# Performance work log

Measured on AMD Instinct MI355X. Metric: run time of the kernel, lower is better.

The kernel has to match this reference:

```python
import jax, jax.numpy as jnp
import numpy as np
from jax import lax

F = 64          # nb_filters
K_DOWN = 4      # size_kernel_sample
K_RES = 3       # size_kernel_res
DIL = 3         # rate_dilation_res
N_DOWN = 3      # downsampling blocks (one level)
N_RES = 4       # residual sub-blocks per block
N_EMB = 512     # codebook size
BETA = 0.25


def conv1d(x, w, b, stride=1, dil=1, act=True):
    # x: (B,T,C), w: (K,Cin,Cout)
    y = lax.conv_general_dilated(x, w, (stride,), 'SAME', rhs_dilation=(dil,),
                                 dimension_numbers=('NWC', 'WIO', 'NWC')) + b
    return jax.nn.relu(y) if act else y


def conv1d_t(x, w, b, stride):
    # transposed conv, w: (K, Cin, Cout)
    y = lax.conv_transpose(x, w, (stride,), 'SAME',
                           dimension_numbers=('NWC', 'WIO', 'NWC')) + b
    return jax.nn.relu(y)


def setup_inputs() -> dict:
    key = jax.random.key(0)
    ks = jax.random.split(key, 12)
    s_in = 1.0 / np.sqrt(K_DOWN * 1)
    s_f = 1.0 / np.sqrt(K_DOWN * F)
    s_r = 1.0 / np.sqrt(K_RES * F)
    return {
        'x': jax.random.normal(ks[0], (4, 65536, 1), dtype=jnp.float32),
        'w_down0': jax.random.normal(ks[1], (K_DOWN, 1, F), dtype=jnp.float32) * s_in,
        'b_down0': jnp.zeros((F,), jnp.float32),
        'w_down': jax.random.normal(ks[2], (N_DOWN - 1, K_DOWN, F, F), dtype=jnp.float32) * s_f,
        'b_down': jnp.zeros((N_DOWN - 1, F), jnp.float32),
        'w_res_enc': jax.random.normal(ks[3], (N_DOWN, N_RES, 2, K_RES, F, F), dtype=jnp.float32) * s_r,
        'b_res_enc': jnp.zeros((N_DOWN, N_RES, 2, F), jnp.float32),
        'codebook': jax.random.normal(ks[4], (N_EMB, F), dtype=jnp.float32),
        'w_res_dec': jax.random.normal(ks[5], (N_DOWN, N_RES, 2, K_RES, F, F), dtype=jnp.float32) * s_r,
        'b_res_dec': jnp.zeros((N_DOWN, N_RES, 2, F), jnp.float32),
        'w_up': jax.random.normal(ks[6], (N_DOWN, K_DOWN, F, F), dtype=jnp.float32) * s_f,
        'b_up': jnp.zeros((N_DOWN, F), jnp.float32),
        'w_proj': jax.random.normal(ks[7], (K_RES, F, 1), dtype=jnp.float32) * s_r,
        'b_proj': jnp.zeros((1,), jnp.float32),
    }


def reference(x, w_down0, b_down0, w_down, b_down, w_res_enc, b_res_enc,
              codebook, w_res_dec, b_res_dec, w_up, b_up, w_proj, b_proj):
    # ---- Encoder: N_DOWN stride-2 downsampling blocks, each followed by
    # N_RES ForwardResidualSubBlocks (dilated conv -> conv, residual add) ----
    h = conv1d(x, w_down0, b_down0, stride=2)
    for blk in range(N_DOWN):
        if blk > 0:
            h = conv1d(h, w_down[blk - 1], b_down[blk - 1], stride=2)
        for r in range(N_RES):
            y = conv1d(h, w_res_enc[blk, r, 0], b_res_enc[blk, r, 0], dil=DIL)
            y = conv1d(y, w_res_enc[blk, r, 1], b_res_enc[blk, r, 1], dil=1)
            h = h + y
    z_e = h  # (B, T/8, F)

    # ---- VectorQuantiser over channel axis ----
    dot = jnp.einsum('btd,kd->btk', z_e, codebook)          # tensordot
    nz = jnp.sum(jnp.square(z_e), axis=-1, keepdims=True)   # (B,T,1)
    ne = jnp.sum(jnp.square(codebook), axis=-1)             # (K,)
    dist = -2.0 * dot + nz + ne                             # squared cdist
    ids = jnp.argmin(dist, axis=-1)                         # (B,T)
    z_q = codebook[ids]                                     # embedding_lookup
    loss_commit = jnp.mean(jnp.linalg.norm(lax.stop_gradient(z_e) - z_q, axis=-1))
    loss_codebook = jnp.mean(jnp.linalg.norm(z_e - lax.stop_gradient(z_q), axis=-1))
    loss_vq = loss_codebook + BETA * loss_commit
    similarity = dot / jnp.sqrt(nz) / jnp.sqrt(ne)

    # ---- Decoder: residual blocks then stride-2 transposed conv, x N_DOWN ----
    h = z_q
    for blk in range(N_DOWN):
        for r in range(N_RES):
            y = conv1d(h, w_res_dec[blk, r, 0], b_res_dec[blk, r, 0], dil=1)
            y = conv1d(y, w_res_dec[blk, r, 1], b_res_dec[blk, r, 1], dil=DIL)
            h = h + y
        h = conv1d_t(h, w_up[blk], b_up[blk], stride=2)
    x_hat = conv1d(h, w_proj, b_proj, act=False)  # linear projection
    return x_hat, loss_vq, ids, similarity
```

## Files before the change

### kernel.cpp

```cpp
#include <hip/hip_runtime.h>
#include <cstdint>


#define OFF_LOSS 262144
#define OFF_IDS  262145
#define OFF_SIM  294913

__global__ __launch_bounds__(256) void down0_kernel(
    const float* __restrict__ x, const float* __restrict__ w,
    const float* __restrict__ bias, float* __restrict__ y)
{
  int idx = blockIdx.x * 256 + threadIdx.x;
  int co = idx & 63;
  int r  = idx >> 6;
  int t  = r & 32767;
  int b  = r >> 15;
  const float* xb = x + (size_t)b * 65536;
  float acc = bias[co];
  #pragma unroll
  for (int k = 0; k < 4; ++k) {
    int gt = 2 * t - 1 + k;
    float xv = ((unsigned)gt < 65536u) ? xb[gt] : 0.f;
    acc += xv * w[k * 64 + co];
  }
  y[(size_t)idx] = fmaxf(acc, 0.f);
}

template <int DIL, bool HAS_RES, int TT>
__global__ __launch_bounds__(512, 8) void conv3_kernel(
    const float* __restrict__ x, const float* __restrict__ w,
    const float* __restrict__ bias, const float* res,
    float* y, int T)
{
  constexpr int TPL = TT / 64;
  constexpr int XT  = TT + 2 * DIL;
  constexpr int XS  = ((XT - 1) | 15) + 1;
  constexpr int NV  = TPL + 2 * DIL;
  __shared__ float xs[64 * XS];
  const int tid  = threadIdx.x;
  const int lane = tid & 63;
  const int b    = blockIdx.y;
  const int t0   = blockIdx.x * TT;
  const int wv   = __builtin_amdgcn_readfirstlane(tid >> 6);
  const int co0  = __builtin_amdgcn_readfirstlane(wv * 8);

  const float* xb = x + (size_t)b * T * 64;
  for (int e = tid; e < 16 * XT; e += 512) {
    int tl = e >> 4, cq = (e & 15) * 4;
    int cs = tl ^ (((cq >> 2) & 7) << 1);
    int gt = t0 - DIL + tl;
    float4 v = make_float4(0.f, 0.f, 0.f, 0.f);
    if ((unsigned)gt < (unsigned)T) v = *(const float4*)&xb[(size_t)gt * 64 + cq];
    xs[(cq + 0) * XS + cs] = v.x;
    xs[(cq + 1) * XS + cs] = v.y;
    xs[(cq + 2) * XS + cs] = v.z;
    xs[(cq + 3) * XS + cs] = v.w;
  }
  __syncthreads();

  float acc[TPL][8] = {};
  const float* wb = w + co0;
  const int tb = TPL * lane;
  for (int ci = 0; ci < 64; ++ci) {
    const int swz = ((ci >> 2) & 7) << 1;
    const float* xr = xs + ci * XS;
    float xv[NV];
    if constexpr (TPL == 2) {
      #pragma unroll
      for (int q = 0; q < NV / 2; ++q) {
        float2 v = *(const float2*)&xr[(tb + 2 * q) ^ swz];
        xv[2*q] = v.x; xv[2*q+1] = v.y;
      }
    } else {
      #pragma unroll
      for (int j = 0; j < NV; ++j) xv[j] = xr[(tb + j) ^ swz];
    }
    const float* w0 = wb + (0 * 64 + ci) * 64;
    const float* w1 = wb + (1 * 64 + ci) * 64;
    const float* w2 = wb + (2 * 64 + ci) * 64;
    #pragma unroll
    for (int j = 0; j < 8; ++j) {
      float c0 = w0[j], c1 = w1[j], c2 = w2[j];
      #pragma unroll
      for (int i = 0; i < TPL; ++i)
        acc[i][j] = fmaf(xv[i], c0, fmaf(xv[i + DIL], c1, fmaf(xv[i + 2 * DIL], c2, acc[i][j])));
    }
  }

  float bs[8];
  #pragma unroll
  for (int j = 0; j < 8; ++j) bs[j] = bias[co0 + j];
  #pragma unroll
  for (int i = 0; i < TPL; ++i) {
    size_t o = ((size_t)b * T + t0 + tb + i) * 64 + co0;
    float r[8];
    #pragma unroll
    for (int j = 0; j < 8; ++j) r[j] = fmaxf(acc[i][j] + bs[j], 0.f);
    if (HAS_RES) {
      float4 v0 = *(const float4*)&res[o];
      float4 v1 = *(const float4*)&res[o + 4];
      r[0] += v0.x; r[1] += v0.y; r[2] += v0.z; r[3] += v0.w;
      r[4] += v1.x; r[5] += v1.y; r[6] += v1.z; r[7] += v1.w;
    }
    *(float4*)&y[o]     = make_float4(r[0], r[1], r[2], r[3]);
    *(float4*)&y[o + 4] = make_float4(r[4], r[5], r[6], r[7]);
  }
}

__global__ __launch_bounds__(512, 8) void down2_kernel(
    const float* __restrict__ x, const float* __restrict__ w,
    const float* __restrict__ bias, float* __restrict__ y, int Tin)
{
  constexpr int XT = 130, XS = 144;
  __shared__ float xs[64 * XS];
  const int tid  = threadIdx.x;
  const int lane = tid & 63;
  const int b    = blockIdx.y;
  const int t0   = blockIdx.x * 64;
  const int Tout = Tin >> 1;
  const int wv   = __builtin_amdgcn_readfirstlane(tid >> 6);
  const int co0  = __builtin_amdgcn_readfirstlane(wv * 8);

  const float* xb = x + (size_t)b * Tin * 64;
  for (int e = tid; e < 16 * XT; e += 512) {
    int tl = e >> 4, cq = (e & 15) * 4;
    int cs = tl ^ (((cq >> 2) & 7) << 1);
    int gt = 2 * t0 - 1 + tl;
    float4 v = make_float4(0.f, 0.f, 0.f, 0.f);
    if ((unsigned)gt < (unsigned)Tin) v = *(const float4*)&xb[(size_t)gt * 64 + cq];
    xs[(cq + 0) * XS + cs] = v.x;
    xs[(cq + 1) * XS + cs] = v.y;
    xs[(cq + 2) * XS + cs] = v.z;
    xs[(cq + 3) * XS + cs] = v.w;
  }
  __syncthreads();

  float acc[8] = {};
  const float* wb = w + co0;
  for (int ci = 0; ci < 64; ++ci) {
    const int swz = ((ci >> 2) & 7) << 1;
    const float* xr = xs + ci * XS;
    float2 v0 = *(const float2*)&xr[(2 * lane) ^ swz];
    float2 v1 = *(const float2*)&xr[(2 * lane + 2) ^ swz];
    float a0 = v0.x, a1 = v0.y, a2 = v1.x, a3 = v1.y;
    const float* w0 = wb + (0 * 64 + ci) * 64;
    const float* w1 = wb + (1 * 64 + ci) * 64;
    const float* w2 = wb + (2 * 64 + ci) * 64;
    const float* w3 = wb + (3 * 64 + ci) * 64;
    #pragma unroll
    for (int j = 0; j < 8; ++j)
      acc[j] = fmaf(a0, w0[j], fmaf(a1, w1[j], fmaf(a2, w2[j], fmaf(a3, w3[j], acc[j]))));
  }

  size_t o = ((size_t)b * Tout + t0 + lane) * 64 + co0;
  #pragma unroll
  for (int q = 0; q < 2; ++q) {
    float4 rr;
    rr.x = fmaxf(acc[4*q+0] + bias[co0 + 4*q+0], 0.f);
    rr.y = fmaxf(acc[4*q+1] + bias[co0 + 4*q+1], 0.f);
    rr.z = fmaxf(acc[4*q+2] + bias[co0 + 4*q+2], 0.f);
    rr.w = fmaxf(acc[4*q+3] + bias[co0 + 4*q+3], 0.f);
    *(float4*)&y[o + 4 * q] = rr;
  }
}

__global__ __launch_bounds__(512, 8) void up_kernel(
    const float* __restrict__ x, const float* __restrict__ w,
    const float* __restrict__ bias, float* __restrict__ y, int Tin)
{
  constexpr int XT = 66, XS = 80;
  __shared__ float xs[64 * XS];
  const int tid  = threadIdx.x;
  const int lane = tid & 63;
  const int b    = blockIdx.y;
  const int u0   = blockIdx.x * 64;
  const int Tout = Tin << 1;
  const int wv   = __builtin_amdgcn_readfirstlane(tid >> 6);
  const int co0  = __builtin_amdgcn_readfirstlane(wv * 8);

  const float* xb = x + (size_t)b * Tin * 64;
  for (int e = tid; e < 16 * XT; e += 512) {
    int ul = e >> 4, cq = (e & 15) * 4;
    int cs = ul ^ (((cq >> 2) & 7) << 1);
    int gu = u0 - 1 + ul;
    float4 v = make_float4(0.f, 0.f, 0.f, 0.f);
    if ((unsigned)gu < (unsigned)Tin) v = *(const float4*)&xb[(size_t)gu * 64 + cq];
    xs[(cq + 0) * XS + cs] = v.x;
    xs[(cq + 1) * XS + cs] = v.y;
    xs[(cq + 2) * XS + cs] = v.z;
    xs[(cq + 3) * XS + cs] = v.w;
  }
  __syncthreads();

  float acce[8] = {}, acco[8] = {};
  const float* wb = w + co0;
  for (int ci = 0; ci < 64; ++ci) {
    const int swz = ((ci >> 2) & 7) << 1;
    const float* xr = xs + ci * XS;
    float a0 = xr[(lane) ^ swz];
    float a1 = xr[(lane + 1) ^ swz];
    float a2 = xr[(lane + 2) ^ swz];
    const float* w0 = wb + (0 * 64 + ci) * 64;
    const float* w1 = wb + (1 * 64 + ci) * 64;
    const float* w2 = wb + (2 * 64 + ci) * 64;
    const float* w3 = wb + (3 * 64 + ci) * 64;
    #pragma unroll
    for (int j = 0; j < 8; ++j) {
      acce[j] = fmaf(a0, w0[j], fmaf(a1, w2[j], acce[j]));
      acco[j] = fmaf(a1, w1[j], fmaf(a2, w3[j], acco[j]));
    }
  }

  size_t oe = ((size_t)b * Tout + 2 * (u0 + lane)) * 64 + co0;
  size_t oo = oe + 64;
  #pragma unroll
  for (int q = 0; q < 2; ++q) {
    float4 re, ro;
    re.x = fmaxf(acce[4*q+0] + bias[co0 + 4*q+0], 0.f);
    re.y = fmaxf(acce[4*q+1] + bias[co0 + 4*q+1], 0.f);
    re.z = fmaxf(acce[4*q+2] + bias[co0 + 4*q+2], 0.f);
    re.w = fmaxf(acce[4*q+3] + bias[co0 + 4*q+3], 0.f);
    ro.x = fmaxf(acco[4*q+0] + bias[co0 + 4*q+0], 0.f);
    ro.y = fmaxf(acco[4*q+1] + bias[co0 + 4*q+1], 0.f);
    ro.z = fmaxf(acco[4*q+2] + bias[co0 + 4*q+2], 0.f);
    ro.w = fmaxf(acco[4*q+3] + bias[co0 + 4*q+3], 0.f);
    *(float4*)&y[oe + 4 * q] = re;
    *(float4*)&y[oo + 4 * q] = ro;
  }
}

__global__ __launch_bounds__(256) void proj_kernel(
    const float* __restrict__ x, const float* __restrict__ w,
    const float* __restrict__ bias, float* __restrict__ out)
{
  const int lane = threadIdx.x & 63;
  const int wid  = (blockIdx.x * 256 + threadIdx.x) >> 6;
  const float w0 = w[lane], w1 = w[64 + lane], w2 = w[128 + lane];
  const float bb = bias[0];
  size_t base = (size_t)wid * 64;
  for (int i = 0; i < 64; ++i) {
    size_t tau = base + i;
    int b = (int)(tau >> 16);
    int t = (int)(tau & 65535);
    const float* xb = x + ((size_t)b * 65536) * 64;
    float pm = (t > 0)     ? xb[(size_t)(t - 1) * 64 + lane] : 0.f;
    float pc =               xb[(size_t)t * 64 + lane];
    float pp = (t < 65535) ? xb[(size_t)(t + 1) * 64 + lane] : 0.f;
    float s = pm * w0 + pc * w1 + pp * w2;
    #pragma unroll
    for (int off = 32; off; off >>= 1) s += __shfl_down(s, off);
    if (lane == 0) out[tau] = s + bb;
  }
}

__global__ __launch_bounds__(256) void nz_kernel(
    const float* __restrict__ ze, float* __restrict__ nz)
{
  int lane = threadIdx.x & 63;
  int tok  = (blockIdx.x * 256 + threadIdx.x) >> 6;
  float v = ze[(size_t)tok * 64 + lane];
  float s = v * v;
  #pragma unroll
  for (int off = 32; off; off >>= 1) s += __shfl_down(s, off);
  if (lane == 0) nz[tok] = s;
}

__global__ __launch_bounds__(256) void ne_kernel(
    const float* __restrict__ cb, float* __restrict__ ne)
{
  int c = blockIdx.x * 256 + threadIdx.x;
  const float4* p = (const float4*)(cb + (size_t)c * 64);
  float s = 0.f;
  #pragma unroll
  for (int q = 0; q < 16; ++q) {
    float4 v = p[q];
    s += v.x * v.x + v.y * v.y + v.z * v.z + v.w * v.w;
  }
  ne[c] = s;
}

__global__ __launch_bounds__(256) void vq_dots_kernel(
    const float* __restrict__ ze, const float* __restrict__ cb,
    const float* __restrict__ nzbuf, const float* __restrict__ nebuf,
    float* __restrict__ sim_out, float2* __restrict__ pmin)
{
  constexpr int ZS = 68, CS = 132;
  __shared__ float zt[64 * ZS];
  __shared__ float ct[64 * CS];
  const int tid = threadIdx.x;
  const int tx  = tid & 15;
  const int ty  = tid >> 4;
  const int bx  = blockIdx.x, by = blockIdx.y;

  {
    const float* zb = ze + (size_t)bx * 64 * 64;
    #pragma unroll
    for (int it = 0; it < 4; ++it) {
      int e = tid + it * 256;
      int tl = e >> 4, cq = (e & 15) * 4;
      int cs = tl ^ (((cq >> 2) & 7) << 2);
      float4 v = *(const float4*)&zb[tl * 64 + cq];
      zt[(cq + 0) * ZS + cs] = v.x;
      zt[(cq + 1) * ZS + cs] = v.y;
      zt[(cq + 2) * ZS + cs] = v.z;
      zt[(cq + 3) * ZS + cs] = v.w;
    }
    const float* cbb = cb + (size_t)by * 128 * 64;
    #pragma unroll
    for (int it = 0; it < 8; ++it) {
      int e = tid + it * 256;
      int el = e >> 4, cq = (e & 15) * 4;
      int cs = el ^ (((cq >> 2) & 7) << 2);
      float4 v = *(const float4*)&cbb[el * 64 + cq];
      ct[(cq + 0) * CS + cs] = v.x;
      ct[(cq + 1) * CS + cs] = v.y;
      ct[(cq + 2) * CS + cs] = v.z;
      ct[(cq + 3) * CS + cs] = v.w;
    }
  }
  __syncthreads();

  float acc[4][8] = {};
  #pragma unroll 4
  for (int k = 0; k < 64; ++k) {
    const int swz = ((k >> 2) & 7) << 2;
    float4 zv = *(const float4*)&zt[k * ZS + ((ty * 4) ^ swz)];
    float4 c0 = *(const float4*)&ct[k * CS + ((tx * 8) ^ swz)];
    float4 c1 = *(const float4*)&ct[k * CS + ((tx * 8 + 4) ^ swz)];
    float zr[4] = {zv.x, zv.y, zv.z, zv.w};
    float cr[8] = {c0.x, c0.y, c0.z, c0.w, c1.x, c1.y, c1.z, c1.w};
    #pragma unroll
    for (int i = 0; i < 4; ++i)
      #pragma unroll
      for (int j = 0; j < 8; ++j)
        acc[i][j] = fmaf(zr[i], cr[j], acc[i][j]);
  }

  float4 nzq = *(const float4*)&nzbuf[bx * 64 + ty * 4];
  float nzv[4] = {nzq.x, nzq.y, nzq.z, nzq.w};
  float4 ne0  = *(const float4*)&nebuf[by * 128 + tx * 8];
  float4 ne1  = *(const float4*)&nebuf[by * 128 + tx * 8 + 4];
  float nev[8]  = {ne0.x, ne0.y, ne0.z, ne0.w, ne1.x, ne1.y, ne1.z, ne1.w};
  float rsne[8];
  #pragma unroll
  for (int j = 0; j < 8; ++j) rsne[j] = 1.f / sqrtf(nev[j]);
  const int ent0 = by * 128 + tx * 8;

  #pragma unroll
  for (int i = 0; i < 4; ++i) {
    const int tok = bx * 64 + ty * 4 + i;
    const float rsnz = 1.f / sqrtf(nzv[i]);
    float dist[8], simv[8];
    #pragma unroll
    for (int j = 0; j < 8; ++j) {
      dist[j] = (-2.f * acc[i][j] + nzv[i]) + nev[j];
      simv[j] = acc[i][j] * rsnz * rsne[j];
    }
    float* so = sim_out + (size_t)tok * 512 + ent0;
    *(float4*)&so[0] = make_float4(simv[0], simv[1], simv[2], simv[3]);
    *(float4*)&so[4] = make_float4(simv[4], simv[5], simv[6], simv[7]);

    float md = dist[0]; int mi = ent0;
    #pragma unroll
    for (int j = 1; j < 8; ++j)
      if (dist[j] < md) { md = dist[j]; mi = ent0 + j; }
    #pragma unroll
    for (int off = 1; off < 16; off <<= 1) {
      float od = __shfl_xor(md, off);
      int   oi = __shfl_xor(mi, off);
      if (od < md || (od == md && oi < mi)) { md = od; mi = oi; }
    }
    if (tx == 0) pmin[tok * 4 + by] = make_float2(md, (float)mi);
  }
}

__global__ __launch_bounds__(256) void vq_finish_kernel(
    const float* __restrict__ ze, const float* __restrict__ cb,
    const float2* __restrict__ pmin, float* __restrict__ zq,
    float* __restrict__ ids_out, float* __restrict__ blocksum)
{
  const int tid = threadIdx.x;
  const int lane = tid & 63, wvid = tid >> 6;
  float lloss = 0.f;
  for (int it = 0; it < 16; ++it) {
    const int tok = blockIdx.x * 64 + wvid * 16 + it;
    float bd = 1e30f; int bi = 0;
    #pragma unroll
    for (int p = 0; p < 4; ++p) {
      float2 pr = pmin[tok * 4 + p];
      float d = pr.x; int i = (int)pr.y;
      if (d < bd || (d == bd && i < bi)) { bd = d; bi = i; }
    }
    float zev = ze[(size_t)tok * 64 + lane];
    float cv  = cb[(size_t)bi * 64 + lane];
    float df = zev - cv;
    float s = df * df;
    #pragma unroll
    for (int off = 32; off; off >>= 1) s += __shfl_down(s, off);
    zq[(size_t)tok * 64 + lane] = cv;
    if (lane == 0) { ids_out[tok] = (float)bi; lloss += sqrtf(s); }
  }
  __shared__ float ls[4];
  if (lane == 0) ls[wvid] = lloss;
  __syncthreads();
  if (tid == 0) blocksum[blockIdx.x] = ls[0] + ls[1] + ls[2] + ls[3];
}

__global__ void loss_fin_kernel(const float* __restrict__ blocksum,
                                float* __restrict__ out)
{
  const int lane = threadIdx.x;
  float s = 0.f;
  for (int i = lane; i < 512; i += 64) s += blocksum[i];
  #pragma unroll
  for (int off = 32; off; off >>= 1) s += __shfl_down(s, off);
  if (lane == 0) out[0] = 1.25f * s / 32768.f;
}

#define LAUNCH_CONV3(DILV, RESV, XP, WP, BP, RP, YP)                           \
  do {                                                                         \
    if (T >= 16384)                                                            \
      conv3_kernel<DILV, RESV, 128><<<dim3(T / 128, 4), 512, 0, stream>>>(     \
          XP, WP, BP, RP, YP, T);                                              \
    else                                                                       \
      conv3_kernel<DILV, RESV, 64><<<dim3(T / 64, 4), 512, 0, stream>>>(       \
          XP, WP, BP, RP, YP, T);                                              \
  } while (0)

extern "C" void kernel_launch(void* const* d_in, const int* in_sizes, int n_in,
                              void* d_out, int out_size, void* d_ws, size_t ws_size,
                              hipStream_t stream)
{
  const float* x       = (const float*)d_in[0];
  const float* w_down0 = (const float*)d_in[1];
  const float* b_down0 = (const float*)d_in[2];
  const float* w_down  = (const float*)d_in[3];
  const float* b_down  = (const float*)d_in[4];
  const float* w_res_e = (const float*)d_in[5];
  const float* b_res_e = (const float*)d_in[6];
  const float* cb      = (const float*)d_in[7];
  const float* w_res_d = (const float*)d_in[8];
  const float* b_res_d = (const float*)d_in[9];
  const float* w_up    = (const float*)d_in[10];
  const float* b_up    = (const float*)d_in[11];
  const float* w_proj  = (const float*)d_in[12];
  const float* b_proj  = (const float*)d_in[13];

  float* out = (float*)d_out;
  const size_t BUF = (size_t)4 * 65536 * 64;
  float*  bufA     = (float*)d_ws;
  float*  bufB     = bufA + BUF;
  float*  nzbuf    = bufB + BUF;
  float*  nebuf    = nzbuf + 32768;
  float2* pmin     = (float2*)(nebuf + 512);
  float*  blocksum = (float*)(pmin + 32768 * 4);

  float* h = bufA;
  float* tmp = bufB;

  down0_kernel<<<32768, 256, 0, stream>>>(x, w_down0, b_down0, h);
  int T = 32768;
  for (int blk = 0; blk < 3; ++blk) {
    if (blk > 0) {
      down2_kernel<<<dim3(T / 2 / 64, 4), 512, 0, stream>>>(
          h, w_down + (size_t)(blk - 1) * 4 * 64 * 64, b_down + (blk - 1) * 64, tmp, T);
      T >>= 1;
      float* s = h; h = tmp; tmp = s;
    }
    for (int r = 0; r < 4; ++r) {
      const float* w0p = w_res_e + (((size_t)blk * 4 + r) * 2 + 0) * 3 * 64 * 64;
      const float* w1p = w_res_e + (((size_t)blk * 4 + r) * 2 + 1) * 3 * 64 * 64;
      const float* b0p = b_res_e + (((size_t)blk * 4 + r) * 2 + 0) * 64;
      const float* b1p = b_res_e + (((size_t)blk * 4 + r) * 2 + 1) * 64;
      LAUNCH_CONV3(3, false, h, w0p, b0p, nullptr, tmp);
      LAUNCH_CONV3(1, true,  tmp, w1p, b1p, h, h);
    }
  }

  nz_kernel<<<8192, 256, 0, stream>>>(h, nzbuf);
  ne_kernel<<<2, 256, 0, stream>>>(cb, nebuf);
  vq_dots_kernel<<<dim3(512, 4), 256, 0, stream>>>(h, cb, nzbuf, nebuf, out + OFF_SIM, pmin);
  vq_finish_kernel<<<512, 256, 0, stream>>>(h, cb, pmin, tmp, out + OFF_IDS, blocksum);
  loss_fin_kernel<<<1, 64, 0, stream>>>(blocksum, out + OFF_LOSS);
  { float* s = h; h = tmp; tmp = s; }

  for (int blk = 0; blk < 3; ++blk) {
    for (int r = 0; r < 4; ++r) {
      const float* w0p = w_res_d + (((size_t)blk * 4 + r) * 2 + 0) * 3 * 64 * 64;
      const float* w1p = w_res_d + (((size_t)blk * 4 + r) * 2 + 1) * 3 * 64 * 64;
      const float* b0p = b_res_d + (((size_t)blk * 4 + r) * 2 + 0) * 64;
      const float* b1p = b_res_d + (((size_t)blk * 4 + r) * 2 + 1) * 64;
      LAUNCH_CONV3(1, false, h, w0p, b0p, nullptr, tmp);
      LAUNCH_CONV3(3, true,  tmp, w1p, b1p, h, h);
    }
    up_kernel<<<dim3(2 * T / 128, 4), 512, 0, stream>>>(
        h, w_up + (size_t)blk * 4 * 64 * 64, b_up + blk * 64, tmp, T);
    T <<= 1;
    float* s = h; h = tmp; tmp = s;
  }

  proj_kernel<<<1024, 256, 0, stream>>>(h, w_proj, b_proj, out);
}
```

Baseline: 1.607 ms.

## Switch encoder activations to channel-major layout for coalesced conv tile loads

```diff
diff --git a/kernel.cpp b/kernel.cpp
--- a/kernel.cpp
+++ b/kernel.cpp
@@ -6,15 +6,13 @@
 #define OFF_IDS  262145
 #define OFF_SIM  294913
 
-__global__ __launch_bounds__(256) void down0_kernel(
+__global__ __launch_bounds__(256) void down0ct_kernel(
     const float* __restrict__ x, const float* __restrict__ w,
     const float* __restrict__ bias, float* __restrict__ y)
 {
-  int idx = blockIdx.x * 256 + threadIdx.x;
-  int co = idx & 63;
-  int r  = idx >> 6;
-  int t  = r & 32767;
-  int b  = r >> 15;
+  const int t  = blockIdx.x * 256 + threadIdx.x;
+  const int co = blockIdx.y;
+  const int b  = blockIdx.z;
   const float* xb = x + (size_t)b * 65536;
   float acc = bias[co];
   #pragma unroll
@@ -23,7 +21,156 @@
     float xv = ((unsigned)gt < 65536u) ? xb[gt] : 0.f;
     acc += xv * w[k * 64 + co];
   }
-  y[(size_t)idx] = fmaxf(acc, 0.f);
+  y[((size_t)b * 64 + co) * 32768 + t] = fmaxf(acc, 0.f);
+}
+
+template <int DIL, bool HAS_RES, int TT>
+__global__ __launch_bounds__(512, 8) void conv3ct_kernel(
+    const float* __restrict__ x, const float* __restrict__ w,
+    const float* __restrict__ bias, const float* res,
+    float* y, int T)
+{
+  constexpr int TPL = TT / 64;
+  constexpr int XT  = TT + 8;
+  constexpr int XS  = ((XT - 1) | 7) + 1;
+  constexpr int NCH = XT / 4;
+  constexpr int NV  = TPL + 2 * DIL;
+  __shared__ float xs[64 * XS];
+  const int tid  = threadIdx.x;
+  const int lane = tid & 63;
+  const int b    = blockIdx.y;
+  const int t0   = blockIdx.x * TT;
+  const int wv   = __builtin_amdgcn_readfirstlane(tid >> 6);
+  const int co0  = __builtin_amdgcn_readfirstlane(wv * 8);
+
+  for (int e = tid; e < 64 * NCH; e += 512) {
+    int row = e / NCH, ch = e - row * NCH;
+    int gt  = t0 - 4 + ch * 4;
+    const float* src = x + ((size_t)b * 64 + row) * T + gt;
+    float4 v;
+    if (gt >= 0 && gt + 3 < T) {
+      v = *(const float4*)src;
+    } else {
+      v.x = ((unsigned)(gt + 0) < (unsigned)T) ? src[0] : 0.f;
+      v.y = ((unsigned)(gt + 1) < (unsigned)T) ? src[1] : 0.f;
+      v.z = ((unsigned)(gt + 2) < (unsigned)T) ? src[2] : 0.f;
+      v.w = ((unsigned)(gt + 3) < (unsigned)T) ? src[3] : 0.f;
+    }
+    *(float4*)&xs[row * XS + ch * 4] = v;
+  }
+  __syncthreads();
+
+  float acc[TPL][8] = {};
+  const float* wb = w + co0;
+  const int tb = TPL * lane;
+  for (int ci = 0; ci < 64; ++ci) {
+    const float* xr = xs + ci * XS;
+    float xv[NV];
+    if constexpr (TPL == 2) {
+      float xq[NV + 2];
+      const int sp = tb + 3 - DIL;
+      #pragma unroll
+      for (int q = 0; q < NV / 2 + 1; ++q) {
+        float2 v = *(const float2*)&xr[sp + 2 * q];
+        xq[2 * q] = v.x; xq[2 * q + 1] = v.y;
+      }
+      #pragma unroll
+      for (int j = 0; j < NV; ++j) xv[j] = xq[j + 1];
+    } else {
+      const int s0 = tb + 4 - DIL;
+      #pragma unroll
+      for (int j = 0; j < NV; ++j) xv[j] = xr[s0 + j];
+    }
+    const float* w0 = wb + (0 * 64 + ci) * 64;
+    const float* w1 = wb + (1 * 64 + ci) * 64;
+    const float* w2 = wb + (2 * 64 + ci) * 64;
+    #pragma unroll
+    for (int j = 0; j < 8; ++j) {
+      float c0 = w0[j], c1 = w1[j], c2 = w2[j];
+      #pragma unroll
+      for (int i = 0; i < TPL; ++i)
+        acc[i][j] = fmaf(xv[i], c0, fmaf(xv[i + DIL], c1, fmaf(xv[i + 2 * DIL], c2, acc[i][j])));
+    }
+  }
+
+  float bs[8];
+  #pragma unroll
+  for (int j = 0; j < 8; ++j) bs[j] = bias[co0 + j];
+  #pragma unroll
+  for (int j = 0; j < 8; ++j) {
+    float rr[TPL];
+    #pragma unroll
+    for (int i = 0; i < TPL; ++i) rr[i] = fmaxf(acc[i][j] + bs[j], 0.f);
+    size_t o = ((size_t)b * 64 + co0 + j) * T + t0 + tb;
+    if (HAS_RES) {
+      if constexpr (TPL == 2) {
+        float2 rv = *(const float2*)&res[o];
+        rr[0] += rv.x; rr[1] += rv.y;
+      } else {
+        rr[0] += res[o];
+      }
+    }
+    if constexpr (TPL == 2) *(float2*)&y[o] = make_float2(rr[0], rr[1]);
+    else                    y[o] = rr[0];
+  }
+}
+
+__global__ __launch_bounds__(512, 8) void down2ct_kernel(
+    const float* __restrict__ x, const float* __restrict__ w,
+    const float* __restrict__ bias, float* __restrict__ y, int Tin)
+{
+  constexpr int XT = 136, XS = 136, NCH = 34;
+  __shared__ float xs[64 * XS];
+  const int tid  = threadIdx.x;
+  const int lane = tid & 63;
+  const int b    = blockIdx.y;
+  const int t0   = blockIdx.x * 64;
+  const int Tout = Tin >> 1;
+  const int wv   = __builtin_amdgcn_readfirstlane(tid >> 6);
+  const int co0  = __builtin_amdgcn_readfirstlane(wv * 8);
+
+  for (int e = tid; e < 64 * NCH; e += 512) {
+    int row = e / NCH, ch = e - row * NCH;
+    int gt  = 2 * t0 - 4 + ch * 4;
+    const float* src = x + ((size_t)b * 64 + row) * Tin + gt;
+    float4 v;
+    if (gt >= 0 && gt + 3 < Tin) {
+      v = *(const float4*)src;
+    } else {
+      v.x = ((unsigned)(gt + 0) < (unsigned)Tin) ? src[0] : 0.f;
+      v.y = ((unsigned)(gt + 1) < (unsigned)Tin) ? src[1] : 0.f;
+      v.z = ((unsigned)(gt + 2) < (unsigned)Tin) ? src[2] : 0.f;
+      v.w = ((unsigned)(gt + 3) < (unsigned)Tin) ? src[3] : 0.f;
+    }
+    *(float4*)&xs[row * XS + ch * 4] = v;
+  }
+  __syncthreads();
+
+  float acc[8] = {};
+  const float* wb = w + co0;
+  for (int ci = 0; ci < 64; ++ci) {
+    const float* xr = xs + ci * XS;
+    float xq[6];
+    #pragma unroll
+    for (int q = 0; q < 3; ++q) {
+      float2 v = *(const float2*)&xr[2 * lane + 2 + 2 * q];
+      xq[2 * q] = v.x; xq[2 * q + 1] = v.y;
+    }
+    float a0 = xq[1], a1 = xq[2], a2 = xq[3], a3 = xq[4];
+    const float* w0 = wb + (0 * 64 + ci) * 64;
+    const float* w1 = wb + (1 * 64 + ci) * 64;
+    const float* w2 = wb + (2 * 64 + ci) * 64;
+    const float* w3 = wb + (3 * 64 + ci) * 64;
+    #pragma unroll
+    for (int j = 0; j < 8; ++j)
+      acc[j] = fmaf(a0, w0[j], fmaf(a1, w1[j], fmaf(a2, w2[j], fmaf(a3, w3[j], acc[j]))));
+  }
+
+  #pragma unroll
+  for (int j = 0; j < 8; ++j) {
+    size_t o = ((size_t)b * 64 + co0 + j) * Tout + t0 + lane;
+    y[o] = fmaxf(acc[j] + bias[co0 + j], 0.f);
+  }
 }
 
 template <int DIL, bool HAS_RES, int TT>
@@ -104,63 +251,6 @@
     }
     *(float4*)&y[o]     = make_float4(r[0], r[1], r[2], r[3]);
     *(float4*)&y[o + 4] = make_float4(r[4], r[5], r[6], r[7]);
-  }
-}
-
-__global__ __launch_bounds__(512, 8) void down2_kernel(
-    const float* __restrict__ x, const float* __restrict__ w,
-    const float* __restrict__ bias, float* __restrict__ y, int Tin)
-{
-  constexpr int XT = 130, XS = 144;
-  __shared__ float xs[64 * XS];
-  const int tid  = threadIdx.x;
-  const int lane = tid & 63;
-  const int b    = blockIdx.y;
-  const int t0   = blockIdx.x * 64;
-  const int Tout = Tin >> 1;
-  const int wv   = __builtin_amdgcn_readfirstlane(tid >> 6);
-  const int co0  = __builtin_amdgcn_readfirstlane(wv * 8);
-
-  const float* xb = x + (size_t)b * Tin * 64;
-  for (int e = tid; e < 16 * XT; e += 512) {
-    int tl = e >> 4, cq = (e & 15) * 4;
-    int cs = tl ^ (((cq >> 2) & 7) << 1);
-    int gt = 2 * t0 - 1 + tl;
-    float4 v = make_float4(0.f, 0.f, 0.f, 0.f);
-    if ((unsigned)gt < (unsigned)Tin) v = *(const float4*)&xb[(size_t)gt * 64 + cq];
-    xs[(cq + 0) * XS + cs] = v.x;
-    xs[(cq + 1) * XS + cs] = v.y;
-    xs[(cq + 2) * XS + cs] = v.z;
-    xs[(cq + 3) * XS + cs] = v.w;
-  }
-  __syncthreads();
-
-  float acc[8] = {};
-  const float* wb = w + co0;
-  for (int ci = 0; ci < 64; ++ci) {
-    const int swz = ((ci >> 2) & 7) << 1;
-    const float* xr = xs + ci * XS;
-    float2 v0 = *(const float2*)&xr[(2 * lane) ^ swz];
-    float2 v1 = *(const float2*)&xr[(2 * lane + 2) ^ swz];
-    float a0 = v0.x, a1 = v0.y, a2 = v1.x, a3 = v1.y;
-    const float* w0 = wb + (0 * 64 + ci) * 64;
-    const float* w1 = wb + (1 * 64 + ci) * 64;
-    const float* w2 = wb + (2 * 64 + ci) * 64;
-    const float* w3 = wb + (3 * 64 + ci) * 64;
-    #pragma unroll
-    for (int j = 0; j < 8; ++j)
-      acc[j] = fmaf(a0, w0[j], fmaf(a1, w1[j], fmaf(a2, w2[j], fmaf(a3, w3[j], acc[j]))));
-  }
-
-  size_t o = ((size_t)b * Tout + t0 + lane) * 64 + co0;
-  #pragma unroll
-  for (int q = 0; q < 2; ++q) {
-    float4 rr;
-    rr.x = fmaxf(acc[4*q+0] + bias[co0 + 4*q+0], 0.f);
-    rr.y = fmaxf(acc[4*q+1] + bias[co0 + 4*q+1], 0.f);
-    rr.z = fmaxf(acc[4*q+2] + bias[co0 + 4*q+2], 0.f);
-    rr.w = fmaxf(acc[4*q+3] + bias[co0 + 4*q+3], 0.f);
-    *(float4*)&y[o + 4 * q] = rr;
   }
 }
 
@@ -258,7 +348,8 @@
 {
   int lane = threadIdx.x & 63;
   int tok  = (blockIdx.x * 256 + threadIdx.x) >> 6;
-  float v = ze[(size_t)tok * 64 + lane];
+  int b = tok >> 13, t = tok & 8191;
+  float v = ze[((size_t)b * 64 + lane) * 8192 + t];
   float s = v * v;
   #pragma unroll
   for (int off = 32; off; off >>= 1) s += __shfl_down(s, off);
@@ -293,17 +384,15 @@
   const int bx  = blockIdx.x, by = blockIdx.y;
 
   {
-    const float* zb = ze + (size_t)bx * 64 * 64;
+    const int bb_ = bx >> 7;
+    const int tr  = (bx & 127) * 64;
+    const float* zb = ze + ((size_t)bb_ * 64) * 8192 + tr;
     #pragma unroll
     for (int it = 0; it < 4; ++it) {
       int e = tid + it * 256;
-      int tl = e >> 4, cq = (e & 15) * 4;
-      int cs = tl ^ (((cq >> 2) & 7) << 2);
-      float4 v = *(const float4*)&zb[tl * 64 + cq];
-      zt[(cq + 0) * ZS + cs] = v.x;
-      zt[(cq + 1) * ZS + cs] = v.y;
-      zt[(cq + 2) * ZS + cs] = v.z;
-      zt[(cq + 3) * ZS + cs] = v.w;
+      int d = e >> 4, ch = (e & 15) * 4;
+      float4 v = *(const float4*)&zb[(size_t)d * 8192 + ch];
+      *(float4*)&zt[d * ZS + ch] = v;
     }
     const float* cbb = cb + (size_t)by * 128 * 64;
     #pragma unroll
@@ -324,7 +413,7 @@
   #pragma unroll 4
   for (int k = 0; k < 64; ++k) {
     const int swz = ((k >> 2) & 7) << 2;
-    float4 zv = *(const float4*)&zt[k * ZS + ((ty * 4) ^ swz)];
+    float4 zv = *(const float4*)&zt[k * ZS + ty * 4];
     float4 c0 = *(const float4*)&ct[k * CS + ((tx * 8) ^ swz)];
     float4 c1 = *(const float4*)&ct[k * CS + ((tx * 8 + 4) ^ swz)];
     float zr[4] = {zv.x, zv.y, zv.z, zv.w};
@@ -391,7 +480,8 @@
       float d = pr.x; int i = (int)pr.y;
       if (d < bd || (d == bd && i < bi)) { bd = d; bi = i; }
     }
-    float zev = ze[(size_t)tok * 64 + lane];
+    const int bb_ = tok >> 13, tt_ = tok & 8191;
+    float zev = ze[((size_t)bb_ * 64 + lane) * 8192 + tt_];
     float cv  = cb[(size_t)bi * 64 + lane];
     float df = zev - cv;
     float s = df * df;
@@ -416,6 +506,16 @@
   for (int off = 32; off; off >>= 1) s += __shfl_down(s, off);
   if (lane == 0) out[0] = 1.25f * s / 32768.f;
 }
+
+#define LAUNCH_CONV3CT(DILV, RESV, XP, WP, BP, RP, YP)                         \
+  do {                                                                         \
+    if (T >= 16384)                                                            \
+      conv3ct_kernel<DILV, RESV, 128><<<dim3(T / 128, 4), 512, 0, stream>>>(   \
+          XP, WP, BP, RP, YP, T);                                              \
+    else                                                                       \
+      conv3ct_kernel<DILV, RESV, 64><<<dim3(T / 64, 4), 512, 0, stream>>>(     \
+          XP, WP, BP, RP, YP, T);                                              \
+  } while (0)
 
 #define LAUNCH_CONV3(DILV, RESV, XP, WP, BP, RP, YP)                           \
   do {                                                                         \
@@ -458,11 +558,11 @@
   float* h = bufA;
   float* tmp = bufB;
 
-  down0_kernel<<<32768, 256, 0, stream>>>(x, w_down0, b_down0, h);
+  down0ct_kernel<<<dim3(128, 64, 4), 256, 0, stream>>>(x, w_down0, b_down0, h);
   int T = 32768;
   for (int blk = 0; blk < 3; ++blk) {
     if (blk > 0) {
-      down2_kernel<<<dim3(T / 2 / 64, 4), 512, 0, stream>>>(
+      down2ct_kernel<<<dim3(T / 2 / 64, 4), 512, 0, stream>>>(
           h, w_down + (size_t)(blk - 1) * 4 * 64 * 64, b_down + (blk - 1) * 64, tmp, T);
       T >>= 1;
       float* s = h; h = tmp; tmp = s;
@@ -472,8 +572,8 @@
       const float* w1p = w_res_e + (((size_t)blk * 4 + r) * 2 + 1) * 3 * 64 * 64;
       const float* b0p = b_res_e + (((size_t)blk * 4 + r) * 2 + 0) * 64;
       const float* b1p = b_res_e + (((size_t)blk * 4 + r) * 2 + 1) * 64;
-      LAUNCH_CONV3(3, false, h, w0p, b0p, nullptr, tmp);
-      LAUNCH_CONV3(1, true,  tmp, w1p, b1p, h, h);
+      LAUNCH_CONV3CT(3, false, h, w0p, b0p, nullptr, tmp);
+      LAUNCH_CONV3CT(1, true,  tmp, w1p, b1p, h, h);
     }
   }
 
```

Result: slower. 1.745 ms (+8.6%).
